# Kernel tuning notes

Hardware: AMD Instinct MI355X
Metric: run time of the kernel (lower is better)

## Reference

```python
import jax, jax.numpy as jnp
import numpy as np

N_NODES = 100000
N_EDGES = 3200000
N_FEAT = 512
N_FILT = 512


def setup_inputs() -> dict:
    key = jax.random.key(0)
    k1, k2, k3, k4, k5 = jax.random.split(key, 5)
    x = jax.random.normal(k1, (N_NODES, N_FEAT), dtype=jnp.float32)
    # xavier_normal_ init for the filter parameter
    std = float(np.sqrt(2.0 / (N_FEAT + N_FILT)))
    filters = jax.random.normal(k2, (N_FEAT, N_FILT), dtype=jnp.float32) * std
    edge_src = jax.random.randint(k3, (N_EDGES,), 0, N_NODES, dtype=jnp.int32)
    edge_dst = jax.random.randint(k4, (N_EDGES,), 0, N_NODES, dtype=jnp.int32)
    edge_weight = jax.random.uniform(k5, (N_EDGES,), dtype=jnp.float32)
    return {"x": x, "filters": filters, "edge_src": edge_src,
            "edge_dst": edge_dst, "edge_weight": edge_weight}


def reference(x, filters, edge_src, edge_dst, edge_weight):
    # Dense feature transform: XF = X @ W   [N, n_filters]
    xf = jnp.matmul(x, filters)
    # Sparse propagation: out[i] = sum_{edges (i<-j)} w_ij * XF[j]
    # transform is COO with rows=edge_dst, cols=edge_src, vals=edge_weight
    msgs = xf[edge_src] * edge_weight[:, None]  # [E, n_filters]
    out = jax.ops.segment_sum(msgs, edge_dst, num_segments=N_NODES)
    return out
```

## Files before the change

### kernel.cpp

```cpp
#include <hip/hip_runtime.h>
#include <hip/hip_bf16.h>
#include <stdint.h>

#define N_NODES 100000
#define N_EDGES 3200000
#define NFEAT   512
#define M_PAD   100096
#define SLOT    80

typedef __attribute__((ext_vector_type(8))) short bf16x8;
typedef __attribute__((ext_vector_type(4))) float f32x4;

using gv_t = const __attribute__((address_space(1))) void;
using lv_t = __attribute__((address_space(3))) void;

__device__ __forceinline__ ushort f2b(float f) {
  uint32_t u = __float_as_uint(f);
  u += 0x7fffu + ((u >> 16) & 1u);
  return (ushort)(u >> 16);
}
__device__ __forceinline__ float b2f(uint32_t lo16) {
  return __uint_as_float(lo16 << 16);
}

__global__ void cvt_x_kernel(const float* __restrict__ x, ushort* __restrict__ xb) {
  const int total4 = M_PAD * NFEAT / 4;
  const int real   = N_NODES * NFEAT;
  for (int i = blockIdx.x * blockDim.x + threadIdx.x; i < total4;
       i += gridDim.x * blockDim.x) {
    int e = i * 4;
    ushort4 o;
    if (e < real) {
      float4 v = *reinterpret_cast<const float4*>(x + e);
      o.x = f2b(v.x); o.y = f2b(v.y); o.z = f2b(v.z); o.w = f2b(v.w);
    } else {
      o = make_ushort4(0, 0, 0, 0);
    }
    *reinterpret_cast<ushort4*>(xb + e) = o;
  }
}

__global__ void cvt_ft_kernel(const float* __restrict__ f, ushort* __restrict__ ftb) {
  int i = blockIdx.x * blockDim.x + threadIdx.x;
  int n = i >> 9, k = i & 511;
  ftb[i] = f2b(f[k * 512 + n]);
}

__global__ __launch_bounds__(256) void gemm_kernel(const ushort* __restrict__ xb,
                                                   const ushort* __restrict__ ftb,
                                                   ushort* __restrict__ xfb) {
  __shared__ ushort As[2][128][32];
  __shared__ ushort Bs[2][128][32];
  const int tid  = threadIdx.x;
  const int lane = tid & 63, wid = tid >> 6;

  const int orig = blockIdx.y * 4 + blockIdx.x;
  const int swz  = (orig & 7) * 391 + (orig >> 3);
  const int bx = swz & 3, by = swz >> 2;

  f32x4 acc[4][4];
#pragma unroll
  for (int i = 0; i < 4; i++)
#pragma unroll
    for (int j = 0; j < 4; j++) acc[i][j] = (f32x4){0.f, 0.f, 0.f, 0.f};

  auto stage = [&](ushort(*lds)[32], const ushort* g, int row0, int k0) {
#pragma unroll
    for (int r = 0; r < 2; ++r) {
      int seg = wid * 2 + r;
      int row = seg * 16 + (lane >> 2);
      int kk  = (lane & 3) * 8;
      const ushort* gp = g + (size_t)(row0 + row) * 512 + (k0 + kk);
      char* lp = (char*)(&lds[0][0]) + seg * 1024;
      __builtin_amdgcn_global_load_lds((gv_t*)gp, (lv_t*)lp, 16, 0, 0);
    }
  };

  stage(As[0], xb, by * 128, 0);
  stage(Bs[0], ftb, bx * 128, 0);
  __syncthreads();

  const int wr = wid >> 1, wc = wid & 1;
  const int m16 = lane & 15, kq = lane >> 4;
  int cur = 0;
  const int NK = NFEAT / 32;
  for (int kt = 0; kt < NK; ++kt) {
    if (kt + 1 < NK) {
      stage(As[cur ^ 1], xb, by * 128, (kt + 1) * 32);
      stage(Bs[cur ^ 1], ftb, bx * 128, (kt + 1) * 32);
    }
    bf16x8 a[4], b[4];
#pragma unroll
    for (int i = 0; i < 4; i++)
      a[i] = *reinterpret_cast<const bf16x8*>(&As[cur][wr * 64 + i * 16 + m16][kq * 8]);
#pragma unroll
    for (int j = 0; j < 4; j++)
      b[j] = *reinterpret_cast<const bf16x8*>(&Bs[cur][wc * 64 + j * 16 + m16][kq * 8]);
#pragma unroll
    for (int i = 0; i < 4; i++)
#pragma unroll
      for (int j = 0; j < 4; j++)
        acc[i][j] = __builtin_amdgcn_mfma_f32_16x16x32_bf16(a[i], b[j], acc[i][j], 0, 0, 0);
    __syncthreads();
    cur ^= 1;
  }

  const size_t rbase = (size_t)by * 128;
  const int cbase = bx * 128;
#pragma unroll
  for (int i = 0; i < 4; i++)
#pragma unroll
    for (int j = 0; j < 4; j++)
#pragma unroll
      for (int r = 0; r < 4; r++) {
        int row = wr * 64 + i * 16 + kq * 4 + r;
        int col = wc * 64 + j * 16 + m16;
        xfb[(rbase + row) * 512 + cbase + col] = f2b(acc[i][j][r]);
      }
}

__global__ void scatter_slot_kernel(const int* __restrict__ src,
                                    const int* __restrict__ dst,
                                    const float* __restrict__ w,
                                    int* __restrict__ cursor,
                                    int2* __restrict__ edges) {
  for (int e = blockIdx.x * blockDim.x + threadIdx.x; e < N_EDGES;
       e += gridDim.x * blockDim.x) {
    int d = dst[e];
    int p = atomicAdd(&cursor[d], 1);
    edges[(size_t)d * SLOT + p] = make_int2(src[e], __float_as_int(w[e]));
  }
}

__global__ __launch_bounds__(256) void spmm_kernel(const ushort* __restrict__ xfb,
                                                   const int* __restrict__ cursor,
                                                   const int2* __restrict__ edges,
                                                   float* __restrict__ out) {
  int node = blockIdx.x * 4 + (threadIdx.x >> 6);
  if (node >= N_NODES) return;
  int lane = threadIdx.x & 63;
  int cnt = cursor[node];
  const int2* ep = edges + (size_t)node * SLOT;
  float acc[8] = {0.f, 0.f, 0.f, 0.f, 0.f, 0.f, 0.f, 0.f};
  for (int e = 0; e < cnt; ++e) {
    int2 ed = ep[e];
    float w = __int_as_float(ed.y);
    uint4 v = *reinterpret_cast<const uint4*>(xfb + (size_t)ed.x * 512 + lane * 8);
    acc[0] += w * b2f(v.x & 0xffffu); acc[1] += w * b2f(v.x >> 16);
    acc[2] += w * b2f(v.y & 0xffffu); acc[3] += w * b2f(v.y >> 16);
    acc[4] += w * b2f(v.z & 0xffffu); acc[5] += w * b2f(v.z >> 16);
    acc[6] += w * b2f(v.w & 0xffffu); acc[7] += w * b2f(v.w >> 16);
  }
  float4 o0 = {acc[0], acc[1], acc[2], acc[3]};
  float4 o1 = {acc[4], acc[5], acc[6], acc[7]};
  float* op = out + (size_t)node * 512 + lane * 8;
  *reinterpret_cast<float4*>(op) = o0;
  *reinterpret_cast<float4*>(op + 4) = o1;
}

extern "C" void kernel_launch(void* const* d_in, const int* in_sizes, int n_in,
                              void* d_out, int out_size, void* d_ws, size_t ws_size,
                              hipStream_t stream) {
  const float* x       = (const float*)d_in[0];
  const float* filters = (const float*)d_in[1];
  const int*   esrc    = (const int*)d_in[2];
  const int*   edst    = (const int*)d_in[3];
  const float* ew      = (const float*)d_in[4];
  float* out = (float*)d_out;

  char* p = (char*)d_ws;
  auto take = [&](size_t b) {
    char* r = p;
    p += (b + 255) & ~(size_t)255;
    return r;
  };
  ushort* xb     = (ushort*)take((size_t)M_PAD * NFEAT * 2);
  ushort* ftb    = (ushort*)take((size_t)NFEAT * NFEAT * 2);
  ushort* xfb    = (ushort*)take((size_t)M_PAD * NFEAT * 2);
  int*    cursor = (int*)take((size_t)N_NODES * 4);

  int2*   edges  = (int2*)xb;

  hipMemsetAsync(cursor, 0, (size_t)N_NODES * 4, stream);
  cvt_x_kernel<<<2048, 256, 0, stream>>>(x, xb);
  cvt_ft_kernel<<<1024, 256, 0, stream>>>(filters, ftb);
  gemm_kernel<<<dim3(4, 782), 256, 0, stream>>>(xb, ftb, xfb);
  scatter_slot_kernel<<<2048, 256, 0, stream>>>(esrc, edst, ew, cursor, edges);
  spmm_kernel<<<(N_NODES + 3) / 4, 256, 0, stream>>>(xfb, cursor, edges, out);
}
```

Before: 774.8 us.

## Fuse x bf16 conversion into GEMM A-load and co-schedule edge scatter blocks

Drops the separate fp32-to-bf16 conversion pass over x. The GEMM now loads fp32 x tiles into registers, converts them, and writes them to LDS, overlapping that with the MFMA work. The edge-bucketing scatter also moves into the same launch as extra blocks, so the atomic scatter can run alongside the GEMM. In exchange, x is read as fp32 four times (once per column block) instead of as bf16, the A path adds register pressure, and the edges buffer now needs its own workspace instead of aliasing xb.

After: 796.2 us. 2.8% more time.

```diff
diff --git a/kernel.cpp b/kernel.cpp
--- a/kernel.cpp
+++ b/kernel.cpp
@@ -8,6 +8,10 @@
 #define M_PAD   100096
 #define SLOT    80
 
+#define GEMM_BLOCKS 3128
+#define SCAT_BLOCKS 1024
+#define TOT_BLOCKS  (GEMM_BLOCKS + SCAT_BLOCKS)
+
 typedef __attribute__((ext_vector_type(8))) short bf16x8;
 typedef __attribute__((ext_vector_type(4))) float f32x4;
 
@@ -23,40 +27,38 @@
   return __uint_as_float(lo16 << 16);
 }
 
-__global__ void cvt_x_kernel(const float* __restrict__ x, ushort* __restrict__ xb) {
-  const int total4 = M_PAD * NFEAT / 4;
-  const int real   = N_NODES * NFEAT;
-  for (int i = blockIdx.x * blockDim.x + threadIdx.x; i < total4;
-       i += gridDim.x * blockDim.x) {
-    int e = i * 4;
-    ushort4 o;
-    if (e < real) {
-      float4 v = *reinterpret_cast<const float4*>(x + e);
-      o.x = f2b(v.x); o.y = f2b(v.y); o.z = f2b(v.z); o.w = f2b(v.w);
-    } else {
-      o = make_ushort4(0, 0, 0, 0);
-    }
-    *reinterpret_cast<ushort4*>(xb + e) = o;
-  }
-}
-
 __global__ void cvt_ft_kernel(const float* __restrict__ f, ushort* __restrict__ ftb) {
   int i = blockIdx.x * blockDim.x + threadIdx.x;
   int n = i >> 9, k = i & 511;
   ftb[i] = f2b(f[k * 512 + n]);
 }
 
-__global__ __launch_bounds__(256) void gemm_kernel(const ushort* __restrict__ xb,
-                                                   const ushort* __restrict__ ftb,
-                                                   ushort* __restrict__ xfb) {
+__global__ __launch_bounds__(256) void fused_gemm_scatter(
+    const float* __restrict__ x, const ushort* __restrict__ ftb,
+    ushort* __restrict__ xfb,
+    const int* __restrict__ esrc, const int* __restrict__ edst,
+    const float* __restrict__ ew, int* __restrict__ cursor,
+    int2* __restrict__ edges) {
   __shared__ ushort As[2][128][32];
   __shared__ ushort Bs[2][128][32];
+
+  if (blockIdx.x >= GEMM_BLOCKS) {
+    for (int e = (blockIdx.x - GEMM_BLOCKS) * 256 + threadIdx.x; e < N_EDGES;
+         e += SCAT_BLOCKS * 256) {
+      int d = edst[e];
+      int p = atomicAdd(&cursor[d], 1);
+      edges[(size_t)d * SLOT + p] = make_int2(esrc[e], __float_as_int(ew[e]));
+    }
+    return;
+  }
+
   const int tid  = threadIdx.x;
   const int lane = tid & 63, wid = tid >> 6;
 
-  const int orig = blockIdx.y * 4 + blockIdx.x;
+  const int orig = blockIdx.x;
   const int swz  = (orig & 7) * 391 + (orig >> 3);
   const int bx = swz & 3, by = swz >> 2;
+  const int row0 = by * 128;
 
   f32x4 acc[4][4];
 #pragma unroll
@@ -64,20 +66,45 @@
 #pragma unroll
     for (int j = 0; j < 4; j++) acc[i][j] = (f32x4){0.f, 0.f, 0.f, 0.f};
 
-  auto stage = [&](ushort(*lds)[32], const ushort* g, int row0, int k0) {
+  auto stageB = [&](int buf, int k0) {
 #pragma unroll
     for (int r = 0; r < 2; ++r) {
       int seg = wid * 2 + r;
       int row = seg * 16 + (lane >> 2);
       int kk  = (lane & 3) * 8;
-      const ushort* gp = g + (size_t)(row0 + row) * 512 + (k0 + kk);
-      char* lp = (char*)(&lds[0][0]) + seg * 1024;
+      const ushort* gp = ftb + (size_t)(bx * 128 + row) * 512 + (k0 + kk);
+      char* lp = (char*)(&Bs[buf][0][0]) + seg * 1024;
       __builtin_amdgcn_global_load_lds((gv_t*)gp, (lv_t*)lp, 16, 0, 0);
     }
   };
 
-  stage(As[0], xb, by * 128, 0);
-  stage(Bs[0], ftb, bx * 128, 0);
+  float4 av[4];
+  auto loadA = [&](int k0) {
+#pragma unroll
+    for (int i = 0; i < 4; ++i) {
+      int flat = i * 256 + tid;
+      int r = flat >> 3, seg = flat & 7;
+      int row = row0 + r;
+      av[i] = (row < N_NODES)
+            ? *reinterpret_cast<const float4*>(x + (size_t)row * 512 + k0 + seg * 4)
+            : make_float4(0.f, 0.f, 0.f, 0.f);
+    }
+  };
+  auto writeA = [&](int buf) {
+#pragma unroll
+    for (int i = 0; i < 4; ++i) {
+      int flat = i * 256 + tid;
+      int r = flat >> 3, seg = flat & 7;
+      ushort4 o;
+      o.x = f2b(av[i].x); o.y = f2b(av[i].y);
+      o.z = f2b(av[i].z); o.w = f2b(av[i].w);
+      *reinterpret_cast<ushort4*>(&As[buf][r][seg * 4]) = o;
+    }
+  };
+
+  loadA(0);
+  stageB(0, 0);
+  writeA(0);
   __syncthreads();
 
   const int wr = wid >> 1, wc = wid & 1;
@@ -86,8 +113,8 @@
   const int NK = NFEAT / 32;
   for (int kt = 0; kt < NK; ++kt) {
     if (kt + 1 < NK) {
-      stage(As[cur ^ 1], xb, by * 128, (kt + 1) * 32);
-      stage(Bs[cur ^ 1], ftb, bx * 128, (kt + 1) * 32);
+      loadA((kt + 1) * 32);
+      stageB(cur ^ 1, (kt + 1) * 32);
     }
     bf16x8 a[4], b[4];
 #pragma unroll
@@ -101,6 +128,7 @@
 #pragma unroll
       for (int j = 0; j < 4; j++)
         acc[i][j] = __builtin_amdgcn_mfma_f32_16x16x32_bf16(a[i], b[j], acc[i][j], 0, 0, 0);
+    if (kt + 1 < NK) writeA(cur ^ 1);
     __syncthreads();
     cur ^= 1;
   }
@@ -117,19 +145,6 @@
         int col = wc * 64 + j * 16 + m16;
         xfb[(rbase + row) * 512 + cbase + col] = f2b(acc[i][j][r]);
       }
-}
-
-__global__ void scatter_slot_kernel(const int* __restrict__ src,
-                                    const int* __restrict__ dst,
-                                    const float* __restrict__ w,
-                                    int* __restrict__ cursor,
-                                    int2* __restrict__ edges) {
-  for (int e = blockIdx.x * blockDim.x + threadIdx.x; e < N_EDGES;
-       e += gridDim.x * blockDim.x) {
-    int d = dst[e];
-    int p = atomicAdd(&cursor[d], 1);
-    edges[(size_t)d * SLOT + p] = make_int2(src[e], __float_as_int(w[e]));
-  }
 }
 
 __global__ __launch_bounds__(256) void spmm_kernel(const ushort* __restrict__ xfb,
@@ -174,17 +189,14 @@
     p += (b + 255) & ~(size_t)255;
     return r;
   };
-  ushort* xb     = (ushort*)take((size_t)M_PAD * NFEAT * 2);
   ushort* ftb    = (ushort*)take((size_t)NFEAT * NFEAT * 2);
   ushort* xfb    = (ushort*)take((size_t)M_PAD * NFEAT * 2);
   int*    cursor = (int*)take((size_t)N_NODES * 4);
-
-  int2*   edges  = (int2*)xb;
+  int2*   edges  = (int2*)take((size_t)N_NODES * SLOT * 8);
 
   hipMemsetAsync(cursor, 0, (size_t)N_NODES * 4, stream);
-  cvt_x_kernel<<<2048, 256, 0, stream>>>(x, xb);
   cvt_ft_kernel<<<1024, 256, 0, stream>>>(filters, ftb);
-  gemm_kernel<<<dim3(4, 782), 256, 0, stream>>>(xb, ftb, xfb);
-  scatter_slot_kernel<<<2048, 256, 0, stream>>>(esrc, edst, ew, cursor, edges);
+  fused_gemm_scatter<<<TOT_BLOCKS, 256, 0, stream>>>(x, ftb, xfb, esrc, edst, ew,
+                                                     cursor, edges);
   spmm_kernel<<<(N_NODES + 3) / 4, 256, 0, stream>>>(xfb, cursor, edges, out);
 }
```
